# Performance work log

Hardware: AMD Instinct MI355X
Metric: run time of the kernel (lower is better)

The kernel has to match this reference:

```python
import jax, jax.numpy as jnp
import numpy as np

N_GROUP, D, DFF = 8, 256, 1024
T = 131072  # total routed tokens


def setup_inputs() -> dict:
    key = jax.random.key(0)
    k_x, k_g, k_u, k_d = jax.random.split(key, 4)
    # kaiming_uniform_(a=sqrt(5)) over fan_in == second-to-last dim
    def kaiming(k, shape, fan_in):
        bound = 1.0 / np.sqrt(fan_in)
        return jax.random.uniform(k, shape, jnp.float32, -bound, bound)
    x = jax.random.normal(k_x, (T, D), jnp.float32)
    weight_gate = kaiming(k_g, (N_GROUP, D, DFF), D)
    weight_up = kaiming(k_u, (N_GROUP, D, DFF), D)
    weight_down = kaiming(k_d, (N_GROUP, DFF, D), DFF)
    # cumulative group end offsets; uniform groups of T // N_GROUP tokens
    offs = (jnp.arange(1, N_GROUP + 1, dtype=jnp.int32) * (T // N_GROUP))
    return {"x": x, "weight_gate": weight_gate, "weight_up": weight_up,
            "weight_down": weight_down, "offs": offs}


def reference(x, weight_gate, weight_up, weight_down, offs):
    # Grouped GLU: for tokens in group g, y = silu(x @ Wg_gate) * (x @ Wg_up) @ Wg_down.
    # offs encodes uniform group boundaries (offs[i] = (i+1)*T/G), so the grouped
    # GEMM is a batched matmul over the expert axis after a reshape.
    G = weight_gate.shape[0]
    t, d = x.shape
    xg = x.reshape(G, t // G, d)                                  # [G, Tg, d]
    z_gate = jnp.einsum('gtd,gdf->gtf', xg, weight_gate)          # [G, Tg, dff]
    z_up = jnp.einsum('gtd,gdf->gtf', xg, weight_up)
    h = jax.nn.silu(z_gate) * z_up
    y = jnp.einsum('gtf,gfd->gtd', h, weight_down)                # [G, Tg, d]
    return y.reshape(t, d)
```

## Files before the change

kernel.cpp:

```cpp
#include <hip/hip_runtime.h>

typedef __bf16 bf16x8 __attribute__((ext_vector_type(8)));
typedef float f32x16 __attribute__((ext_vector_type(16)));
typedef unsigned int u32x4 __attribute__((ext_vector_type(4)));

#define NGROUP 8
#define DMODEL 256
#define DFF    1024
#define TTOT   131072
#define TGRP   (TTOT / NGROUP)
#define MTILE  256
#define NCHUNK 32

__device__ __forceinline__ unsigned int f2bf(float f) {
    unsigned int x = __builtin_bit_cast(unsigned int, f);
    return (x + 0x7fffu + ((x >> 16) & 1u)) >> 16;
}
__device__ __forceinline__ unsigned int pack2(float lo, float hi) {
    return f2bf(lo) | (f2bf(hi) << 16);
}

__device__ __forceinline__ void g2l(const void* g, void* l) {
    __builtin_amdgcn_global_load_lds(
        (const __attribute__((address_space(1))) unsigned int*)g,
        (__attribute__((address_space(3))) unsigned int*)l, 16, 0, 0);
}

__global__ void k_cvt_x(const float4* __restrict__ in, u32x4* __restrict__ out) {
    int t = blockIdx.x * 256 + threadIdx.x;
    float4 a = in[2 * t];
    float4 b = in[2 * t + 1];
    u32x4 v = { pack2(a.x, a.y), pack2(a.z, a.w), pack2(b.x, b.y), pack2(b.z, b.w) };
    out[t] = v;
}

__global__ void k_prep_w(const float* __restrict__ wg, const float* __restrict__ wu,
                         const float* __restrict__ wd, u32x4* __restrict__ out) {
    int t = blockIdx.x * 256 + threadIdx.x;
    int lane = t & 63;
    int q = lane >> 5, l31 = lane & 31;
    int fg = t >> 6;
    int fid = fg % 48;
    int gc  = fg / 48;
    int c = gc & 31, g = gc >> 5;
    const float* src;
    int stride;
    if (fid < 32) {
        const float* w = (fid < 16) ? wg : wu;
        int ks = fid & 15;
        src = w + (size_t)(g * 256 + ks * 16 + q * 8) * 1024 + c * 32 + l31;
        stride = 1024;
    } else {
        int idx = fid - 32;
        int ks2 = idx >> 3, nb = idx & 7;
        src = wd + (size_t)(g * 1024 + (c * 2 + ks2) * 16 + q * 8) * 256 + nb * 32 + l31;
        stride = 256;
    }
    u32x4 v = { pack2(src[0],          src[stride]),
                pack2(src[2 * stride], src[3 * stride]),
                pack2(src[4 * stride], src[5 * stride]),
                pack2(src[6 * stride], src[7 * stride]) };
    out[t] = v;
}

__global__ __launch_bounds__(512, 2)
void k_glu(const u32x4* __restrict__ xb,
           const u32x4* __restrict__ wcomb,
           float* __restrict__ y) {
    __shared__ u32x4 smem[4096];

    const int tid  = threadIdx.x;
    const int lane = tid & 63;
    const int w    = tid >> 6;
    const int q    = lane >> 5;
    const int l31  = lane & 31;

    const int g    = blockIdx.x & 7;
    const int m0   = g * TGRP + (blockIdx.x >> 3) * MTILE;
    const int tokw = w * 32 + l31;

    u32x4 xf[16];
    {
        const u32x4* xrow = xb + (size_t)(m0 + tokw) * 32 + q;
        #pragma unroll
        for (int ks = 0; ks < 16; ++ks) xf[ks] = xrow[ks * 2];
    }

    f32x16 acc[8];
    #pragma unroll
    for (int nb = 0; nb < 8; ++nb)
        #pragma unroll
        for (int i = 0; i < 16; ++i) acc[nb][i] = 0.0f;

    const u32x4* wcg = wcomb + (size_t)(g * 32) * 3072;
    const unsigned int sw = ((l31 >> 2) & 3) << 4;
    char* hrow = (char*)smem + 49152 + w * 2048 + l31 * 64;

    for (int c = 0; c < NCHUNK; ++c) {
        __syncthreads();
        {
            const u32x4* gsrc = wcg + (size_t)c * 3072;
            #pragma unroll
            for (int i = 0; i < 6; ++i) {
                int off = i * 512 + w * 64;
                g2l(gsrc + off + lane, smem + off);
            }
        }
        __syncthreads();

        f32x16 zg, zu;
        #pragma unroll
        for (int i = 0; i < 16; ++i) { zg[i] = 0.0f; zu[i] = 0.0f; }
        #pragma unroll
        for (int ks = 0; ks < 16; ++ks) {
            const u32x4 a1 = smem[ks * 64 + lane];
            const u32x4 a2 = smem[1024 + ks * 64 + lane];
            zg = __builtin_amdgcn_mfma_f32_32x32x16_bf16(
                     __builtin_bit_cast(bf16x8, a1),
                     __builtin_bit_cast(bf16x8, xf[ks]), zg, 0, 0, 0);
            zu = __builtin_amdgcn_mfma_f32_32x32x16_bf16(
                     __builtin_bit_cast(bf16x8, a2),
                     __builtin_bit_cast(bf16x8, xf[ks]), zu, 0, 0, 0);
        }

        #pragma unroll
        for (int a = 0; a < 4; ++a) {
            const float g0 = zg[4 * a + 0], g1 = zg[4 * a + 1];
            const float g2 = zg[4 * a + 2], g3 = zg[4 * a + 3];
            const float h0 = g0 / (1.0f + __expf(-g0)) * zu[4 * a + 0];
            const float h1 = g1 / (1.0f + __expf(-g1)) * zu[4 * a + 1];
            const float h2 = g2 / (1.0f + __expf(-g2)) * zu[4 * a + 2];
            const float h3 = g3 / (1.0f + __expf(-g3)) * zu[4 * a + 3];
            uint2 pv;
            pv.x = pack2(h0, h1);
            pv.y = pack2(h2, h3);
            *(uint2*)(hrow + ((unsigned)(a * 16 + q * 8) ^ sw)) = pv;
        }

        #pragma unroll
        for (int ks2 = 0; ks2 < 2; ++ks2) {
            const u32x4 ha = *(const u32x4*)(hrow + ((unsigned)(ks2 * 32 + q * 16) ^ sw));
            #pragma unroll
            for (int nb = 0; nb < 8; ++nb) {
                const u32x4 bd = smem[2048 + (ks2 * 8 + nb) * 64 + lane];
                acc[nb] = __builtin_amdgcn_mfma_f32_32x32x16_bf16(
                              __builtin_bit_cast(bf16x8, ha),
                              __builtin_bit_cast(bf16x8, bd), acc[nb], 0, 0, 0);
            }
        }
    }

    float* yp = y + (size_t)(m0 + w * 32) * DMODEL;
    #pragma unroll
    for (int nb = 0; nb < 8; ++nb) {
        const int col = nb * 32 + l31;
        #pragma unroll
        for (int r = 0; r < 16; ++r) {
            const int row = (r & 3) + (r >> 2) * 8 + q * 4;
            yp[(size_t)row * DMODEL + col] = acc[nb][r];
        }
    }
}

extern "C" void kernel_launch(void* const* d_in, const int* in_sizes, int n_in,
                              void* d_out, int out_size, void* d_ws, size_t ws_size,
                              hipStream_t stream) {
    const float* x  = (const float*)d_in[0];
    const float* wg = (const float*)d_in[1];
    const float* wu = (const float*)d_in[2];
    const float* wd = (const float*)d_in[3];
    float* y = (float*)d_out;

    u32x4* xb    = (u32x4*)d_ws;
    u32x4* wcomb = xb + 4194304;

    k_cvt_x<<<dim3(TTOT * DMODEL / 8 / 256), dim3(256), 0, stream>>>((const float4*)x, xb);
    k_prep_w<<<dim3(3072), dim3(256), 0, stream>>>(wg, wu, wd, wcomb);
    k_glu<<<dim3(512), dim3(512), 0, stream>>>(xb, wcomb, y);
}
```

Measured before the change: 483.7 us.

## Fuse x conversion into GLU kernel, double tokens per wave, prefetch weights

Removes the separate fp32-to-bf16 conversion pass over x by loading fp32 x directly in the GLU kernel and packing it in registers. Each wave now handles two 32-token tiles with half as many threads per block, so every weight fragment read from LDS feeds twice as many MFMAs. The h intermediate is moved between lanes with cross-lane shuffles instead of a round trip through LDS. Weight chunks are prefetched in two phases overlapped with compute. The cost is much higher register pressure from doubled accumulators and x fragments, which could cause spills or lower occupancy.

```diff
diff --git a/kernel.cpp b/kernel.cpp
--- a/kernel.cpp
+++ b/kernel.cpp
@@ -19,20 +19,13 @@
 __device__ __forceinline__ unsigned int pack2(float lo, float hi) {
     return f2bf(lo) | (f2bf(hi) << 16);
 }
-
 __device__ __forceinline__ void g2l(const void* g, void* l) {
     __builtin_amdgcn_global_load_lds(
         (const __attribute__((address_space(1))) unsigned int*)g,
         (__attribute__((address_space(3))) unsigned int*)l, 16, 0, 0);
 }
-
-__global__ void k_cvt_x(const float4* __restrict__ in, u32x4* __restrict__ out) {
-    int t = blockIdx.x * 256 + threadIdx.x;
-    float4 a = in[2 * t];
-    float4 b = in[2 * t + 1];
-    u32x4 v = { pack2(a.x, a.y), pack2(a.z, a.w), pack2(b.x, b.y), pack2(b.z, b.w) };
-    out[t] = v;
-}
+#define MFMA(A, B, C) __builtin_amdgcn_mfma_f32_32x32x16_bf16( \
+        __builtin_bit_cast(bf16x8, (A)), __builtin_bit_cast(bf16x8, (B)), (C), 0, 0, 0)
 
 __global__ void k_prep_w(const float* __restrict__ wg, const float* __restrict__ wu,
                          const float* __restrict__ wd, u32x4* __restrict__ out) {
@@ -63,11 +56,11 @@
     out[t] = v;
 }
 
-__global__ __launch_bounds__(512, 2)
-void k_glu(const u32x4* __restrict__ xb,
+__global__ __launch_bounds__(256, 2)
+void k_glu(const float* __restrict__ x,
            const u32x4* __restrict__ wcomb,
            float* __restrict__ y) {
-    __shared__ u32x4 smem[4096];
+    __shared__ u32x4 smem[3072];
 
     const int tid  = threadIdx.x;
     const int lane = tid & 63;
@@ -77,87 +70,139 @@
 
     const int g    = blockIdx.x & 7;
     const int m0   = g * TGRP + (blockIdx.x >> 3) * MTILE;
-    const int tokw = w * 32 + l31;
-
-    u32x4 xf[16];
+
+    const u32x4* wcg = wcomb + (size_t)g * (NCHUNK * 3072);
+
     {
-        const u32x4* xrow = xb + (size_t)(m0 + tokw) * 32 + q;
-        #pragma unroll
-        for (int ks = 0; ks < 16; ++ks) xf[ks] = xrow[ks * 2];
-    }
-
-    f32x16 acc[8];
+        const u32x4* src = wcg;
+        #pragma unroll
+        for (int i = 0; i < 8; ++i) {
+            int off = i * 256 + w * 64;
+            g2l(src + off + lane, smem + off);
+        }
+        #pragma unroll
+        for (int i = 0; i < 4; ++i) {
+            int off = 2048 + i * 256 + w * 64;
+            g2l(src + off + lane, smem + off);
+        }
+    }
+
+    u32x4 xf[2][16];
     #pragma unroll
-    for (int nb = 0; nb < 8; ++nb)
-        #pragma unroll
-        for (int i = 0; i < 16; ++i) acc[nb][i] = 0.0f;
-
-    const u32x4* wcg = wcomb + (size_t)(g * 32) * 3072;
-    const unsigned int sw = ((l31 >> 2) & 3) << 4;
-    char* hrow = (char*)smem + 49152 + w * 2048 + l31 * 64;
+    for (int t = 0; t < 2; ++t) {
+        const float* rowp = x + (size_t)(m0 + (w * 2 + t) * 32 + l31) * DMODEL + q * 8;
+        #pragma unroll
+        for (int ks = 0; ks < 16; ++ks) {
+            float4 a = *(const float4*)(rowp + ks * 16);
+            float4 b = *(const float4*)(rowp + ks * 16 + 4);
+            u32x4 v = { pack2(a.x, a.y), pack2(a.z, a.w), pack2(b.x, b.y), pack2(b.z, b.w) };
+            xf[t][ks] = v;
+        }
+    }
+
+    f32x16 acc[2][8];
+    #pragma unroll
+    for (int t = 0; t < 2; ++t)
+        #pragma unroll
+        for (int nb = 0; nb < 8; ++nb)
+            #pragma unroll
+            for (int i = 0; i < 16; ++i) acc[t][nb][i] = 0.0f;
+
+    __syncthreads();
 
     for (int c = 0; c < NCHUNK; ++c) {
-        __syncthreads();
-        {
-            const u32x4* gsrc = wcg + (size_t)c * 3072;
-            #pragma unroll
-            for (int i = 0; i < 6; ++i) {
-                int off = i * 512 + w * 64;
-                g2l(gsrc + off + lane, smem + off);
-            }
-        }
-        __syncthreads();
-
-        f32x16 zg, zu;
-        #pragma unroll
-        for (int i = 0; i < 16; ++i) { zg[i] = 0.0f; zu[i] = 0.0f; }
+        f32x16 zg[2], zu[2];
+        #pragma unroll
+        for (int t = 0; t < 2; ++t)
+            #pragma unroll
+            for (int i = 0; i < 16; ++i) { zg[t][i] = 0.0f; zu[t][i] = 0.0f; }
         #pragma unroll
         for (int ks = 0; ks < 16; ++ks) {
             const u32x4 a1 = smem[ks * 64 + lane];
             const u32x4 a2 = smem[1024 + ks * 64 + lane];
-            zg = __builtin_amdgcn_mfma_f32_32x32x16_bf16(
-                     __builtin_bit_cast(bf16x8, a1),
-                     __builtin_bit_cast(bf16x8, xf[ks]), zg, 0, 0, 0);
-            zu = __builtin_amdgcn_mfma_f32_32x32x16_bf16(
-                     __builtin_bit_cast(bf16x8, a2),
-                     __builtin_bit_cast(bf16x8, xf[ks]), zu, 0, 0, 0);
-        }
-
-        #pragma unroll
-        for (int a = 0; a < 4; ++a) {
-            const float g0 = zg[4 * a + 0], g1 = zg[4 * a + 1];
-            const float g2 = zg[4 * a + 2], g3 = zg[4 * a + 3];
-            const float h0 = g0 / (1.0f + __expf(-g0)) * zu[4 * a + 0];
-            const float h1 = g1 / (1.0f + __expf(-g1)) * zu[4 * a + 1];
-            const float h2 = g2 / (1.0f + __expf(-g2)) * zu[4 * a + 2];
-            const float h3 = g3 / (1.0f + __expf(-g3)) * zu[4 * a + 3];
-            uint2 pv;
-            pv.x = pack2(h0, h1);
-            pv.y = pack2(h2, h3);
-            *(uint2*)(hrow + ((unsigned)(a * 16 + q * 8) ^ sw)) = pv;
+            zg[0] = MFMA(a1, xf[0][ks], zg[0]);
+            zg[1] = MFMA(a1, xf[1][ks], zg[1]);
+            zu[0] = MFMA(a2, xf[0][ks], zu[0]);
+            zu[1] = MFMA(a2, xf[1][ks], zu[1]);
+        }
+
+        unsigned int pv[2][8];
+        #pragma unroll
+        for (int t = 0; t < 2; ++t) {
+            #pragma unroll
+            for (int a = 0; a < 4; ++a) {
+                const float g0 = zg[t][4 * a + 0], g1 = zg[t][4 * a + 1];
+                const float g2 = zg[t][4 * a + 2], g3 = zg[t][4 * a + 3];
+                const float h0 = g0 / (1.0f + __expf(-g0)) * zu[t][4 * a + 0];
+                const float h1 = g1 / (1.0f + __expf(-g1)) * zu[t][4 * a + 1];
+                const float h2 = g2 / (1.0f + __expf(-g2)) * zu[t][4 * a + 2];
+                const float h3 = g3 / (1.0f + __expf(-g3)) * zu[t][4 * a + 3];
+                pv[t][2 * a]     = pack2(h0, h1);
+                pv[t][2 * a + 1] = pack2(h2, h3);
+            }
+        }
+
+        u32x4 hf[2][2];
+        #pragma unroll
+        for (int t = 0; t < 2; ++t) {
+            const int s0[4] = {2, 3, 6, 7};
+            const int s1[4] = {0, 1, 4, 5};
+            unsigned int rr[4];
+            #pragma unroll
+            for (int i = 0; i < 4; ++i) {
+                unsigned int s = q ? pv[t][s1[i]] : pv[t][s0[i]];
+                rr[i] = (unsigned int)__shfl_xor((int)s, 32, 64);
+            }
+            u32x4 h0 = { q ? rr[0] : pv[t][0], q ? rr[1] : pv[t][1],
+                         q ? pv[t][2] : rr[0], q ? pv[t][3] : rr[1] };
+            u32x4 h1 = { q ? rr[2] : pv[t][4], q ? rr[3] : pv[t][5],
+                         q ? pv[t][6] : rr[2], q ? pv[t][7] : rr[3] };
+            hf[t][0] = h0;
+            hf[t][1] = h1;
+        }
+
+        __syncthreads();
+        if (c + 1 < NCHUNK) {
+            const u32x4* src = wcg + (size_t)(c + 1) * 3072;
+            #pragma unroll
+            for (int i = 0; i < 8; ++i) {
+                int off = i * 256 + w * 64;
+                g2l(src + off + lane, smem + off);
+            }
         }
 
         #pragma unroll
         for (int ks2 = 0; ks2 < 2; ++ks2) {
-            const u32x4 ha = *(const u32x4*)(hrow + ((unsigned)(ks2 * 32 + q * 16) ^ sw));
             #pragma unroll
             for (int nb = 0; nb < 8; ++nb) {
                 const u32x4 bd = smem[2048 + (ks2 * 8 + nb) * 64 + lane];
-                acc[nb] = __builtin_amdgcn_mfma_f32_32x32x16_bf16(
-                              __builtin_bit_cast(bf16x8, ha),
-                              __builtin_bit_cast(bf16x8, bd), acc[nb], 0, 0, 0);
-            }
-        }
-    }
-
-    float* yp = y + (size_t)(m0 + w * 32) * DMODEL;
+                acc[0][nb] = MFMA(hf[0][ks2], bd, acc[0][nb]);
+                acc[1][nb] = MFMA(hf[1][ks2], bd, acc[1][nb]);
+            }
+        }
+
+        __syncthreads();
+        if (c + 1 < NCHUNK) {
+            const u32x4* src = wcg + (size_t)(c + 1) * 3072;
+            #pragma unroll
+            for (int i = 0; i < 4; ++i) {
+                int off = 2048 + i * 256 + w * 64;
+                g2l(src + off + lane, smem + off);
+            }
+        }
+    }
+
     #pragma unroll
-    for (int nb = 0; nb < 8; ++nb) {
-        const int col = nb * 32 + l31;
-        #pragma unroll
-        for (int r = 0; r < 16; ++r) {
-            const int row = (r & 3) + (r >> 2) * 8 + q * 4;
-            yp[(size_t)row * DMODEL + col] = acc[nb][r];
+    for (int t = 0; t < 2; ++t) {
+        float* yp = y + (size_t)(m0 + (w * 2 + t) * 32) * DMODEL;
+        #pragma unroll
+        for (int nb = 0; nb < 8; ++nb) {
+            const int col = nb * 32 + l31;
+            #pragma unroll
+            for (int r = 0; r < 16; ++r) {
+                const int row = (r & 3) + (r >> 2) * 8 + q * 4;
+                yp[(size_t)row * DMODEL + col] = acc[t][nb][r];
+            }
         }
     }
 }
@@ -171,10 +216,8 @@
     const float* wd = (const float*)d_in[3];
     float* y = (float*)d_out;
 
-    u32x4* xb    = (u32x4*)d_ws;
-    u32x4* wcomb = xb + 4194304;
-
-    k_cvt_x<<<dim3(TTOT * DMODEL / 8 / 256), dim3(256), 0, stream>>>((const float4*)x, xb);
+    u32x4* wcomb = (u32x4*)d_ws;
+
     k_prep_w<<<dim3(3072), dim3(256), 0, stream>>>(wg, wu, wd, wcomb);
-    k_glu<<<dim3(512), dim3(512), 0, stream>>>(xb, wcomb, y);
-}
+    k_glu<<<dim3(512), dim3(256), 0, stream>>>(x, wcomb, y);
+}
```

Result: slower. 1.863 ms (+285.1%).
